# Kernel tuning notes

Measured on AMD Instinct MI355X. Metric: run time of the kernel, lower is better.

Reference implementation:

```python
import jax, jax.numpy as jnp
import numpy as np

N_ENTITIES = 100000
N_RELATIONS = 64
EMBED_DIM = 128
BATCH = 16384
KG_L2_LAMBDA = 1e-05


def setup_inputs() -> dict:
    key = jax.random.key(0)
    ks = jax.random.split(key, 8)
    d = EMBED_DIM
    scale = 1.0 / np.sqrt(d)  # xavier-ish init scale
    return {
        'h': jax.random.randint(ks[0], (BATCH,), 0, N_ENTITIES),
        'r': jax.random.randint(ks[1], (BATCH,), 0, N_RELATIONS),
        'pos_t': jax.random.randint(ks[2], (BATCH,), 0, N_ENTITIES),
        'neg_t': jax.random.randint(ks[3], (BATCH,), 0, N_ENTITIES),
        'entity_embed': jax.random.normal(ks[4], (N_ENTITIES, d), jnp.float32) * scale,
        'relation_embed': jax.random.normal(ks[5], (N_RELATIONS, d), jnp.float32) * scale,
        'h_trans_w1': jnp.ones((d,), jnp.float32),
        'h_trans_w2': jnp.ones((d,), jnp.float32),
        'h_bias_b': jnp.zeros((d,), jnp.float32),
        'r_trans_w1': jnp.ones((d,), jnp.float32),
        'r_trans_w2': jnp.ones((d,), jnp.float32),
        'r_bias_b': jnp.zeros((d,), jnp.float32),
        'sem_trans_w': jax.random.normal(ks[6], (2 * d, d), jnp.float32) * scale,
    }


def _l2_loss_mean(x):
    return jnp.mean(jnp.sum(x * x, axis=1) / 2.0)


def reference(h, r, pos_t, neg_t, entity_embed, relation_embed,
              h_trans_w1, h_trans_w2, h_bias_b,
              r_trans_w1, r_trans_w2, r_bias_b, sem_trans_w):
    h_e = entity_embed[h]          # (B, d)
    r_e = relation_embed[r]        # (B, d)
    pos_t_e = entity_embed[pos_t]  # (B, d)
    neg_t_e = entity_embed[neg_t]  # (B, d)

    # calc_sur: sem[b,i,j] = h_e[b,i] * r_e[b,j]; matmul(sem, w) == h_e * (r_e @ w),
    # matmul(sem^T, w) == r_e * (h_e @ w). Fused form of the same math.
    r_w1 = (r_e @ h_trans_w1)[:, None]
    r_w2 = (r_e @ h_trans_w2)[:, None]
    h_w1 = (h_e @ r_trans_w1)[:, None]
    h_w2 = (h_e @ r_trans_w2)[:, None]
    cross_h = h_e * r_w1 + r_e * h_w2 + h_bias_b  # (B, d)
    cross_r = h_e * r_w2 + r_e * h_w1 + r_bias_b  # (B, d)

    pred_t = jnp.concatenate([cross_h, cross_r], axis=1) @ sem_trans_w  # (B, d)
    pos_score = jnp.sum(pred_t * pos_t_e, axis=1)
    neg_score = jnp.sum(pred_t * neg_t_e, axis=1)
    # -logsigmoid(x) == softplus(-x)
    kg_loss = jnp.mean(jax.nn.softplus(-(pos_score - neg_score)))
    l2_loss = (_l2_loss_mean(cross_h) + _l2_loss_mean(cross_r)
               + _l2_loss_mean(pos_t_e) + _l2_loss_mean(neg_t_e))
    return kg_loss + KG_L2_LAMBDA * l2_loss
```

## Files before the change

### kernel.cpp

```cpp
#include <hip/hip_runtime.h>
#include <hip/hip_bf16.h>

#define B_TOTAL 16384
#define EMB 128
#define NBLK 256
#define TPB 256
#define KG_LAMBDA 1e-5f
#define WT_STRIDE 264
#define IMG_BYTES 73728
#define IMG_DW (IMG_BYTES / 4)
#define WT_DW 16896
#define SVEC_BYTE_OFF 67584

typedef float f32x4 __attribute__((ext_vector_type(4)));
typedef unsigned u32x4 __attribute__((ext_vector_type(4)));
typedef __bf16 bf16x8 __attribute__((ext_vector_type(8)));

__device__ __forceinline__ unsigned pack_bf16x2(float a, float b) {
  unsigned ua = __float_as_uint(a);
  unsigned ub = __float_as_uint(b);
  ua = (ua + 0x7fffu + ((ua >> 16) & 1u)) >> 16;
  ub = (ub + 0x7fffu + ((ub >> 16) & 1u)) >> 16;
  return ua | (ub << 16);
}

__global__ __launch_bounds__(256) void sur_prep(
    const float* __restrict__ W,
    const float* __restrict__ htw1, const float* __restrict__ htw2,
    const float* __restrict__ hbias,
    const float* __restrict__ rtw1, const float* __restrict__ rtw2,
    const float* __restrict__ rbias,
    unsigned* __restrict__ img) {
  const int idx = blockIdx.x * 256 + threadIdx.x;
  if (idx < WT_DW) {
    const int c = idx / 132;
    const int kp = idx - c * 132;
    unsigned v = 0;
    if (kp < 128) {
      const float f0 = W[(2 * kp) * EMB + c];
      const float f1 = W[(2 * kp + 1) * EMB + c];
      v = pack_bf16x2(f0, f1);
    }
    img[idx] = v;
  } else {
    const int j = idx - WT_DW;
    float val = 0.f;
    if (j < 768) {
      const int vsel = j >> 7, cc = j & 127;
      const float* src = vsel == 0 ? htw1 : vsel == 1 ? htw2 : vsel == 2 ? hbias
                       : vsel == 3 ? rtw1 : vsel == 4 ? rtw2 : rbias;
      val = src[cc];
    }
    img[idx] = __float_as_uint(val);
  }
}

__global__ __launch_bounds__(TPB, 2) void sur_fused(
    const int* __restrict__ h, const int* __restrict__ r,
    const int* __restrict__ pos_t, const int* __restrict__ neg_t,
    const float* __restrict__ ent, const float* __restrict__ rel,
    const unsigned* __restrict__ img, float* __restrict__ out) {
  __shared__ __align__(16) unsigned char smem[IMG_BYTES];
  __shared__ float redbuf[2][4];
  unsigned short (*Wt)[WT_STRIDE] = (unsigned short(*)[WT_STRIDE])smem;
  const float* svec = (const float*)(smem + SVEC_BYTE_OFF);

  const int tid = threadIdx.x;
  const int lane = tid & 63;
  const int wave = tid >> 6;
  const int ri = lane & 15;
  const int q = lane >> 4;

  const int rowbase = blockIdx.x * 64 + wave * 16;
  const int hidx = h[rowbase + ri] * EMB;
  const int ridx = r[rowbase + ri] * EMB;
  int pidx[4], nidx[4];
  #pragma unroll
  for (int g = 0; g < 4; ++g) {
    pidx[g] = pos_t[rowbase + q * 4 + g] * EMB;
    nidx[g] = neg_t[rowbase + q * 4 + g] * EMB;
  }

  {
    const float4* gsrc = (const float4*)img;
    float4* ldst = (float4*)smem;
    #pragma unroll
    for (int i = 0; i < IMG_BYTES / 16 / TPB; ++i)
      ldst[i * TPB + tid] = gsrc[i * TPB + tid];
  }

  float he[4][8], re[4][8];
  #pragma unroll
  for (int kt = 0; kt < 4; ++kt) {
    const int c0 = kt * 32 + q * 8;
    const float4 a0 = *reinterpret_cast<const float4*>(ent + hidx + c0);
    const float4 a1 = *reinterpret_cast<const float4*>(ent + hidx + c0 + 4);
    const float4 b0 = *reinterpret_cast<const float4*>(rel + ridx + c0);
    const float4 b1 = *reinterpret_cast<const float4*>(rel + ridx + c0 + 4);
    he[kt][0] = a0.x; he[kt][1] = a0.y; he[kt][2] = a0.z; he[kt][3] = a0.w;
    he[kt][4] = a1.x; he[kt][5] = a1.y; he[kt][6] = a1.z; he[kt][7] = a1.w;
    re[kt][0] = b0.x; re[kt][1] = b0.y; re[kt][2] = b0.z; re[kt][3] = b0.w;
    re[kt][4] = b1.x; re[kt][5] = b1.y; re[kt][6] = b1.z; re[kt][7] = b1.w;
  }

  float pe[4][8], ne[4][8];
  #pragma unroll
  for (int g = 0; g < 4; ++g) {
    #pragma unroll
    for (int n = 0; n < 8; ++n) {
      pe[g][n] = ent[pidx[g] + n * 16 + ri];
      ne[g][n] = ent[nidx[g] + n * 16 + ri];
    }
  }

  __syncthreads();

  float prw1 = 0.f, prw2 = 0.f, phw1 = 0.f, phw2 = 0.f;
  #pragma unroll
  for (int kt = 0; kt < 4; ++kt) {
    const int c0 = kt * 32 + q * 8;
    #pragma unroll
    for (int j = 0; j < 8; ++j) {
      prw1 = fmaf(re[kt][j], svec[0 * 128 + c0 + j], prw1);
      prw2 = fmaf(re[kt][j], svec[1 * 128 + c0 + j], prw2);
      phw1 = fmaf(he[kt][j], svec[3 * 128 + c0 + j], phw1);
      phw2 = fmaf(he[kt][j], svec[4 * 128 + c0 + j], phw2);
    }
  }
  prw1 += __shfl_xor(prw1, 16); prw2 += __shfl_xor(prw2, 16);
  phw1 += __shfl_xor(phw1, 16); phw2 += __shfl_xor(phw2, 16);
  prw1 += __shfl_xor(prw1, 32); prw2 += __shfl_xor(prw2, 32);
  phw1 += __shfl_xor(phw1, 32); phw2 += __shfl_xor(phw2, 32);

  float acc_l2 = 0.f;
  u32x4 afu[8];
  #pragma unroll
  for (int kt = 0; kt < 4; ++kt) {
    const int c0 = kt * 32 + q * 8;
    float ch[8], cr[8];
    #pragma unroll
    for (int j = 0; j < 8; ++j) {
      const float hb = svec[2 * 128 + c0 + j];
      const float rb = svec[5 * 128 + c0 + j];
      ch[j] = fmaf(he[kt][j], prw1, fmaf(re[kt][j], phw2, hb));
      cr[j] = fmaf(he[kt][j], prw2, fmaf(re[kt][j], phw1, rb));
      acc_l2 += ch[j] * ch[j] + cr[j] * cr[j];
    }
    #pragma unroll
    for (int d = 0; d < 4; ++d) {
      afu[kt][d]     = pack_bf16x2(ch[2 * d], ch[2 * d + 1]);
      afu[kt + 4][d] = pack_bf16x2(cr[2 * d], cr[2 * d + 1]);
    }
  }

  f32x4 acc[8];
  #pragma unroll
  for (int n = 0; n < 8; ++n) acc[n] = 0.f;
  #pragma unroll
  for (int t = 0; t < 8; ++t) {
    const bf16x8 av = __builtin_bit_cast(bf16x8, afu[t]);
    #pragma unroll
    for (int n = 0; n < 8; ++n) {
      const bf16x8 bv = *reinterpret_cast<const bf16x8*>(&Wt[n * 16 + ri][t * 32 + q * 8]);
      acc[n] = __builtin_amdgcn_mfma_f32_16x16x32_bf16(av, bv, acc[n], 0, 0, 0);
    }
  }

  float sp[4] = {0.f, 0.f, 0.f, 0.f}, sn[4] = {0.f, 0.f, 0.f, 0.f};
  #pragma unroll
  for (int n = 0; n < 8; ++n) {
    #pragma unroll
    for (int g = 0; g < 4; ++g) {
      sp[g] = fmaf(acc[n][g], pe[g][n], sp[g]);
      sn[g] = fmaf(acc[n][g], ne[g][n], sn[g]);
      acc_l2 += pe[g][n] * pe[g][n] + ne[g][n] * ne[g][n];
    }
  }
  #pragma unroll
  for (int m = 1; m < 16; m <<= 1) {
    #pragma unroll
    for (int g = 0; g < 4; ++g) {
      sp[g] += __shfl_xor(sp[g], m);
      sn[g] += __shfl_xor(sn[g], m);
    }
  }
  float acc_kg = 0.f;
  if (ri == 0) {
    #pragma unroll
    for (int g = 0; g < 4; ++g) {
      const float x = sn[g] - sp[g];
      acc_kg += fmaxf(x, 0.f) + log1pf(expf(-fabsf(x)));
    }
  }

  float kg = acc_kg, l2 = acc_l2;
  #pragma unroll
  for (int m = 1; m < 64; m <<= 1) {
    kg += __shfl_xor(kg, m);
    l2 += __shfl_xor(l2, m);
  }
  if (lane == 0) { redbuf[0][wave] = kg; redbuf[1][wave] = l2; }
  __syncthreads();
  if (tid == 0) {
    const float K = redbuf[0][0] + redbuf[0][1] + redbuf[0][2] + redbuf[0][3];
    const float L = redbuf[1][0] + redbuf[1][1] + redbuf[1][2] + redbuf[1][3];
    atomicAdd(out, (K + KG_LAMBDA * 0.5f * L) * (1.0f / (float)B_TOTAL));
  }
}

extern "C" void kernel_launch(void* const* d_in, const int* in_sizes, int n_in,
                              void* d_out, int out_size, void* d_ws, size_t ws_size,
                              hipStream_t stream) {
  const int* h     = (const int*)d_in[0];
  const int* r     = (const int*)d_in[1];
  const int* pos_t = (const int*)d_in[2];
  const int* neg_t = (const int*)d_in[3];
  const float* ent  = (const float*)d_in[4];
  const float* rel  = (const float*)d_in[5];
  const float* htw1 = (const float*)d_in[6];
  const float* htw2 = (const float*)d_in[7];
  const float* hb   = (const float*)d_in[8];
  const float* rtw1 = (const float*)d_in[9];
  const float* rtw2 = (const float*)d_in[10];
  const float* rb   = (const float*)d_in[11];
  const float* W    = (const float*)d_in[12];
  unsigned* img = (unsigned*)d_ws;
  float* out = (float*)d_out;

  hipMemsetAsync(d_out, 0, sizeof(float), stream);
  hipLaunchKernelGGL(sur_prep, dim3(IMG_DW / 256), dim3(256), 0, stream,
                     W, htw1, htw2, hb, rtw1, rtw2, rb, img);
  hipLaunchKernelGGL(sur_fused, dim3(NBLK), dim3(TPB), 0, stream,
                     h, r, pos_t, neg_t, ent, rel, img, out);
}
```

Baseline: 116.1 us.

## Pre-swizzle weight fragments in global memory and halve rows per wave

The prep kernel now writes the bf16 weight matrix already arranged in per-lane MFMA B-fragment order. The fused kernel reads these fragments directly from global/L2 instead of staging a 72KB shared-memory image behind a barrier. Each wave now handles 8 rows instead of 16, with duplicated rows masked out of the loss sums, and the grid doubles to 512 blocks for more parallelism. The output memset is folded into the prep kernel, removing one launch. In exchange, half of the MFMA rows are redundant and every block re-reads the weights from cache.

```diff
diff --git a/kernel.cpp b/kernel.cpp
--- a/kernel.cpp
+++ b/kernel.cpp
@@ -3,14 +3,13 @@
 
 #define B_TOTAL 16384
 #define EMB 128
-#define NBLK 256
 #define TPB 256
+#define NBLK 512
 #define KG_LAMBDA 1e-5f
-#define WT_STRIDE 264
-#define IMG_BYTES 73728
-#define IMG_DW (IMG_BYTES / 4)
-#define WT_DW 16896
-#define SVEC_BYTE_OFF 67584
+#define FRAG_DW 16384
+#define SVEC_DW 768
+#define IMG_DW (FRAG_DW + SVEC_DW)
+#define PREP_BLOCKS (IMG_DW / 256)
 
 typedef float f32x4 __attribute__((ext_vector_type(4)));
 typedef unsigned u32x4 __attribute__((ext_vector_type(4)));
@@ -30,28 +29,28 @@
     const float* __restrict__ hbias,
     const float* __restrict__ rtw1, const float* __restrict__ rtw2,
     const float* __restrict__ rbias,
-    unsigned* __restrict__ img) {
+    unsigned* __restrict__ img, float* __restrict__ out) {
   const int idx = blockIdx.x * 256 + threadIdx.x;
-  if (idx < WT_DW) {
-    const int c = idx / 132;
-    const int kp = idx - c * 132;
-    unsigned v = 0;
-    if (kp < 128) {
-      const float f0 = W[(2 * kp) * EMB + c];
-      const float f1 = W[(2 * kp + 1) * EMB + c];
-      v = pack_bf16x2(f0, f1);
-    }
-    img[idx] = v;
+  if (idx < FRAG_DW) {
+    const int kp = idx >> 7;
+    const int c  = idx & 127;
+    const float f0 = W[(2 * kp) * EMB + c];
+    const float f1 = W[(2 * kp + 1) * EMB + c];
+    const int t  = kp >> 4;
+    const int rm = kp & 15;
+    const int q8 = rm >> 2;
+    const int w  = rm & 3;
+    const int n  = c >> 4;
+    const int ri = c & 15;
+    const int l  = q8 * 16 + ri;
+    img[((t * 8 + n) << 8) + (l << 2) + w] = pack_bf16x2(f0, f1);
   } else {
-    const int j = idx - WT_DW;
-    float val = 0.f;
-    if (j < 768) {
-      const int vsel = j >> 7, cc = j & 127;
-      const float* src = vsel == 0 ? htw1 : vsel == 1 ? htw2 : vsel == 2 ? hbias
-                       : vsel == 3 ? rtw1 : vsel == 4 ? rtw2 : rbias;
-      val = src[cc];
-    }
-    img[idx] = __float_as_uint(val);
+    const int j = idx - FRAG_DW;
+    const int vsel = j >> 7, cc = j & 127;
+    const float* src = vsel == 0 ? htw1 : vsel == 1 ? htw2 : vsel == 2 ? hbias
+                     : vsel == 3 ? rtw1 : vsel == 4 ? rtw2 : rbias;
+    img[idx] = __float_as_uint(src[cc]);
+    if (j == 0) out[0] = 0.f;
   }
 }
 
@@ -60,10 +59,7 @@
     const int* __restrict__ pos_t, const int* __restrict__ neg_t,
     const float* __restrict__ ent, const float* __restrict__ rel,
     const unsigned* __restrict__ img, float* __restrict__ out) {
-  __shared__ __align__(16) unsigned char smem[IMG_BYTES];
   __shared__ float redbuf[2][4];
-  unsigned short (*Wt)[WT_STRIDE] = (unsigned short(*)[WT_STRIDE])smem;
-  const float* svec = (const float*)(smem + SVEC_BYTE_OFF);
 
   const int tid = threadIdx.x;
   const int lane = tid & 63;
@@ -71,23 +67,20 @@
   const int ri = lane & 15;
   const int q = lane >> 4;
 
-  const int rowbase = blockIdx.x * 64 + wave * 16;
-  const int hidx = h[rowbase + ri] * EMB;
-  const int ridx = r[rowbase + ri] * EMB;
+  const int rowbase = (blockIdx.x * 4 + wave) * 8;
+  const int arow = ri & 7;
+  const int hidx = h[rowbase + arow] * EMB;
+  const int ridx = r[rowbase + arow] * EMB;
+  const int qq = q & 1;
   int pidx[4], nidx[4];
   #pragma unroll
   for (int g = 0; g < 4; ++g) {
-    pidx[g] = pos_t[rowbase + q * 4 + g] * EMB;
-    nidx[g] = neg_t[rowbase + q * 4 + g] * EMB;
-  }
-
-  {
-    const float4* gsrc = (const float4*)img;
-    float4* ldst = (float4*)smem;
-    #pragma unroll
-    for (int i = 0; i < IMG_BYTES / 16 / TPB; ++i)
-      ldst[i * TPB + tid] = gsrc[i * TPB + tid];
-  }
+    const int rr = rowbase + qq * 4 + g;
+    pidx[g] = pos_t[rr] * EMB;
+    nidx[g] = neg_t[rr] * EMB;
+  }
+
+  const float* svec = (const float*)(img + FRAG_DW);
 
   float he[4][8], re[4][8];
   #pragma unroll
@@ -103,28 +96,24 @@
     re[kt][4] = b1.x; re[kt][5] = b1.y; re[kt][6] = b1.z; re[kt][7] = b1.w;
   }
 
-  float pe[4][8], ne[4][8];
-  #pragma unroll
-  for (int g = 0; g < 4; ++g) {
-    #pragma unroll
-    for (int n = 0; n < 8; ++n) {
-      pe[g][n] = ent[pidx[g] + n * 16 + ri];
-      ne[g][n] = ent[nidx[g] + n * 16 + ri];
-    }
-  }
-
-  __syncthreads();
-
   float prw1 = 0.f, prw2 = 0.f, phw1 = 0.f, phw2 = 0.f;
   #pragma unroll
   for (int kt = 0; kt < 4; ++kt) {
     const int c0 = kt * 32 + q * 8;
-    #pragma unroll
-    for (int j = 0; j < 8; ++j) {
-      prw1 = fmaf(re[kt][j], svec[0 * 128 + c0 + j], prw1);
-      prw2 = fmaf(re[kt][j], svec[1 * 128 + c0 + j], prw2);
-      phw1 = fmaf(he[kt][j], svec[3 * 128 + c0 + j], phw1);
-      phw2 = fmaf(he[kt][j], svec[4 * 128 + c0 + j], phw2);
+    const float4 w1a = *reinterpret_cast<const float4*>(svec + 0 * 128 + c0);
+    const float4 w1b = *reinterpret_cast<const float4*>(svec + 0 * 128 + c0 + 4);
+    const float4 w2a = *reinterpret_cast<const float4*>(svec + 1 * 128 + c0);
+    const float4 w2b = *reinterpret_cast<const float4*>(svec + 1 * 128 + c0 + 4);
+    const float4 v1a = *reinterpret_cast<const float4*>(svec + 3 * 128 + c0);
+    const float4 v1b = *reinterpret_cast<const float4*>(svec + 3 * 128 + c0 + 4);
+    const float4 v2a = *reinterpret_cast<const float4*>(svec + 4 * 128 + c0);
+    const float4 v2b = *reinterpret_cast<const float4*>(svec + 4 * 128 + c0 + 4);
+    #pragma unroll
+    for (int j = 0; j < 4; ++j) {
+      prw1 = fmaf(re[kt][j], (&w1a.x)[j], prw1); prw1 = fmaf(re[kt][j + 4], (&w1b.x)[j], prw1);
+      prw2 = fmaf(re[kt][j], (&w2a.x)[j], prw2); prw2 = fmaf(re[kt][j + 4], (&w2b.x)[j], prw2);
+      phw1 = fmaf(he[kt][j], (&v1a.x)[j], phw1); phw1 = fmaf(he[kt][j + 4], (&v1b.x)[j], phw1);
+      phw2 = fmaf(he[kt][j], (&v2a.x)[j], phw2); phw2 = fmaf(he[kt][j + 4], (&v2b.x)[j], phw2);
     }
   }
   prw1 += __shfl_xor(prw1, 16); prw2 += __shfl_xor(prw2, 16);
@@ -132,19 +121,24 @@
   prw1 += __shfl_xor(prw1, 32); prw2 += __shfl_xor(prw2, 32);
   phw1 += __shfl_xor(phw1, 32); phw2 += __shfl_xor(phw2, 32);
 
+  const float m8 = (ri < 8) ? 1.f : 0.f;
   float acc_l2 = 0.f;
   u32x4 afu[8];
   #pragma unroll
   for (int kt = 0; kt < 4; ++kt) {
     const int c0 = kt * 32 + q * 8;
+    const float4 hba = *reinterpret_cast<const float4*>(svec + 2 * 128 + c0);
+    const float4 hbb = *reinterpret_cast<const float4*>(svec + 2 * 128 + c0 + 4);
+    const float4 rba = *reinterpret_cast<const float4*>(svec + 5 * 128 + c0);
+    const float4 rbb = *reinterpret_cast<const float4*>(svec + 5 * 128 + c0 + 4);
     float ch[8], cr[8];
     #pragma unroll
     for (int j = 0; j < 8; ++j) {
-      const float hb = svec[2 * 128 + c0 + j];
-      const float rb = svec[5 * 128 + c0 + j];
+      const float hb = j < 4 ? (&hba.x)[j] : (&hbb.x)[j - 4];
+      const float rb = j < 4 ? (&rba.x)[j] : (&rbb.x)[j - 4];
       ch[j] = fmaf(he[kt][j], prw1, fmaf(re[kt][j], phw2, hb));
       cr[j] = fmaf(he[kt][j], prw2, fmaf(re[kt][j], phw1, rb));
-      acc_l2 += ch[j] * ch[j] + cr[j] * cr[j];
+      acc_l2 = fmaf(m8, ch[j] * ch[j] + cr[j] * cr[j], acc_l2);
     }
     #pragma unroll
     for (int d = 0; d < 4; ++d) {
@@ -153,6 +147,17 @@
     }
   }
 
+  float pe[4][8], ne[4][8];
+  #pragma unroll
+  for (int g = 0; g < 4; ++g) {
+    #pragma unroll
+    for (int n = 0; n < 8; ++n) {
+      pe[g][n] = ent[pidx[g] + n * 16 + ri];
+      ne[g][n] = ent[nidx[g] + n * 16 + ri];
+    }
+  }
+
+  const u32x4* frag = (const u32x4*)img;
   f32x4 acc[8];
   #pragma unroll
   for (int n = 0; n < 8; ++n) acc[n] = 0.f;
@@ -161,11 +166,12 @@
     const bf16x8 av = __builtin_bit_cast(bf16x8, afu[t]);
     #pragma unroll
     for (int n = 0; n < 8; ++n) {
-      const bf16x8 bv = *reinterpret_cast<const bf16x8*>(&Wt[n * 16 + ri][t * 32 + q * 8]);
+      const bf16x8 bv = __builtin_bit_cast(bf16x8, frag[(t * 8 + n) * 64 + lane]);
       acc[n] = __builtin_amdgcn_mfma_f32_16x16x32_bf16(av, bv, acc[n], 0, 0, 0);
     }
   }
 
+  const float mq = (q < 2) ? 1.f : 0.f;
   float sp[4] = {0.f, 0.f, 0.f, 0.f}, sn[4] = {0.f, 0.f, 0.f, 0.f};
   #pragma unroll
   for (int n = 0; n < 8; ++n) {
@@ -173,7 +179,7 @@
     for (int g = 0; g < 4; ++g) {
       sp[g] = fmaf(acc[n][g], pe[g][n], sp[g]);
       sn[g] = fmaf(acc[n][g], ne[g][n], sn[g]);
-      acc_l2 += pe[g][n] * pe[g][n] + ne[g][n] * ne[g][n];
+      acc_l2 = fmaf(mq, pe[g][n] * pe[g][n] + ne[g][n] * ne[g][n], acc_l2);
     }
   }
   #pragma unroll
@@ -185,7 +191,7 @@
     }
   }
   float acc_kg = 0.f;
-  if (ri == 0) {
+  if (ri == 0 && q < 2) {
     #pragma unroll
     for (int g = 0; g < 4; ++g) {
       const float x = sn[g] - sp[g];
@@ -227,9 +233,8 @@
   unsigned* img = (unsigned*)d_ws;
   float* out = (float*)d_out;
 
-  hipMemsetAsync(d_out, 0, sizeof(float), stream);
-  hipLaunchKernelGGL(sur_prep, dim3(IMG_DW / 256), dim3(256), 0, stream,
-                     W, htw1, htw2, hb, rtw1, rtw2, rb, img);
+  hipLaunchKernelGGL(sur_prep, dim3(PREP_BLOCKS), dim3(256), 0, stream,
+                     W, htw1, htw2, hb, rtw1, rtw2, rb, img, out);
   hipLaunchKernelGGL(sur_fused, dim3(NBLK), dim3(TPB), 0, stream,
                      h, r, pos_t, neg_t, ent, rel, img, out);
 }
```

After: 121.2 us. 1.04x slower.

## Halve rows per wave, stage pred in LDS, vectorize tail gathers, fold memset

Applied to the files above, without the earlier changes.

Each wave now handles 8 rows instead of 16. The MFMA runs on duplicated rows and the duplicates are masked out of the L2 sum. The block count doubles so more of the GPU's compute units are busy. Pred tiles are written to shared memory so each lane can load pos/neg entity rows as coalesced float4 segments instead of scalar strided loads. The separate memset is folded into the prep kernel. In exchange, half of the MFMA work is wasted, more shared-memory weight-image copies are made, and extra barriers are added.

```diff
diff --git a/kernel.cpp b/kernel.cpp
--- a/kernel.cpp
+++ b/kernel.cpp
@@ -3,14 +3,15 @@
 
 #define B_TOTAL 16384
 #define EMB 128
-#define NBLK 256
 #define TPB 256
+#define NBLK 512
 #define KG_LAMBDA 1e-5f
 #define WT_STRIDE 264
 #define IMG_BYTES 73728
 #define IMG_DW (IMG_BYTES / 4)
 #define WT_DW 16896
 #define SVEC_BYTE_OFF 67584
+#define PREDL_STRIDE 132
 
 typedef float f32x4 __attribute__((ext_vector_type(4)));
 typedef unsigned u32x4 __attribute__((ext_vector_type(4)));
@@ -30,7 +31,7 @@
     const float* __restrict__ hbias,
     const float* __restrict__ rtw1, const float* __restrict__ rtw2,
     const float* __restrict__ rbias,
-    unsigned* __restrict__ img) {
+    unsigned* __restrict__ img, float* __restrict__ out) {
   const int idx = blockIdx.x * 256 + threadIdx.x;
   if (idx < WT_DW) {
     const int c = idx / 132;
@@ -52,6 +53,7 @@
       val = src[cc];
     }
     img[idx] = __float_as_uint(val);
+    if (j == 0) out[0] = 0.f;
   }
 }
 
@@ -64,22 +66,22 @@
   __shared__ float redbuf[2][4];
   unsigned short (*Wt)[WT_STRIDE] = (unsigned short(*)[WT_STRIDE])smem;
   const float* svec = (const float*)(smem + SVEC_BYTE_OFF);
+  float* predL = (float*)smem;
 
   const int tid = threadIdx.x;
   const int lane = tid & 63;
   const int wave = tid >> 6;
   const int ri = lane & 15;
   const int q = lane >> 4;
-
-  const int rowbase = blockIdx.x * 64 + wave * 16;
-  const int hidx = h[rowbase + ri] * EMB;
-  const int ridx = r[rowbase + ri] * EMB;
-  int pidx[4], nidx[4];
-  #pragma unroll
-  for (int g = 0; g < 4; ++g) {
-    pidx[g] = pos_t[rowbase + q * 4 + g] * EMB;
-    nidx[g] = neg_t[rowbase + q * 4 + g] * EMB;
-  }
+  const int erow = lane >> 3;
+  const int eseg = lane & 7;
+
+  const int rowbase = (blockIdx.x * 4 + wave) * 8;
+  const int arow = ri & 7;
+  const int hidx = h[rowbase + arow] * EMB;
+  const int ridx = r[rowbase + arow] * EMB;
+  const int pp = pos_t[rowbase + erow] * EMB;
+  const int nn = neg_t[rowbase + erow] * EMB;
 
   {
     const float4* gsrc = (const float4*)img;
@@ -103,16 +105,6 @@
     re[kt][4] = b1.x; re[kt][5] = b1.y; re[kt][6] = b1.z; re[kt][7] = b1.w;
   }
 
-  float pe[4][8], ne[4][8];
-  #pragma unroll
-  for (int g = 0; g < 4; ++g) {
-    #pragma unroll
-    for (int n = 0; n < 8; ++n) {
-      pe[g][n] = ent[pidx[g] + n * 16 + ri];
-      ne[g][n] = ent[nidx[g] + n * 16 + ri];
-    }
-  }
-
   __syncthreads();
 
   float prw1 = 0.f, prw2 = 0.f, phw1 = 0.f, phw2 = 0.f;
@@ -132,6 +124,7 @@
   prw1 += __shfl_xor(prw1, 32); prw2 += __shfl_xor(prw2, 32);
   phw1 += __shfl_xor(phw1, 32); phw2 += __shfl_xor(phw2, 32);
 
+  const float m8 = (ri < 8) ? 1.f : 0.f;
   float acc_l2 = 0.f;
   u32x4 afu[8];
   #pragma unroll
@@ -144,7 +137,7 @@
       const float rb = svec[5 * 128 + c0 + j];
       ch[j] = fmaf(he[kt][j], prw1, fmaf(re[kt][j], phw2, hb));
       cr[j] = fmaf(he[kt][j], prw2, fmaf(re[kt][j], phw1, rb));
-      acc_l2 += ch[j] * ch[j] + cr[j] * cr[j];
+      acc_l2 = fmaf(m8, ch[j] * ch[j] + cr[j] * cr[j], acc_l2);
     }
     #pragma unroll
     for (int d = 0; d < 4; ++d) {
@@ -166,31 +159,46 @@
     }
   }
 
-  float sp[4] = {0.f, 0.f, 0.f, 0.f}, sn[4] = {0.f, 0.f, 0.f, 0.f};
-  #pragma unroll
-  for (int n = 0; n < 8; ++n) {
-    #pragma unroll
-    for (int g = 0; g < 4; ++g) {
-      sp[g] = fmaf(acc[n][g], pe[g][n], sp[g]);
-      sn[g] = fmaf(acc[n][g], ne[g][n], sn[g]);
-      acc_l2 += pe[g][n] * pe[g][n] + ne[g][n] * ne[g][n];
-    }
-  }
-  #pragma unroll
-  for (int m = 1; m < 16; m <<= 1) {
-    #pragma unroll
-    for (int g = 0; g < 4; ++g) {
-      sp[g] += __shfl_xor(sp[g], m);
-      sn[g] += __shfl_xor(sn[g], m);
-    }
-  }
+  float4 pe4[4], ne4[4];
+  #pragma unroll
+  for (int j = 0; j < 4; ++j) {
+    pe4[j] = *reinterpret_cast<const float4*>(ent + pp + eseg * 16 + j * 4);
+    ne4[j] = *reinterpret_cast<const float4*>(ent + nn + eseg * 16 + j * 4);
+  }
+
+  __syncthreads();
+
+  float* myPred = predL + wave * (8 * PREDL_STRIDE);
+  if (q < 2) {
+    #pragma unroll
+    for (int n = 0; n < 8; ++n) {
+      #pragma unroll
+      for (int g = 0; g < 4; ++g)
+        myPred[(q * 4 + g) * PREDL_STRIDE + n * 16 + ri] = acc[n][g];
+    }
+  }
+  __syncthreads();
+
+  float sp = 0.f, sn = 0.f;
+  #pragma unroll
+  for (int j = 0; j < 4; ++j) {
+    const float4 pr = *reinterpret_cast<const float4*>(
+        myPred + erow * PREDL_STRIDE + eseg * 16 + j * 4);
+    sp += pr.x * pe4[j].x + pr.y * pe4[j].y + pr.z * pe4[j].z + pr.w * pe4[j].w;
+    sn += pr.x * ne4[j].x + pr.y * ne4[j].y + pr.z * ne4[j].z + pr.w * ne4[j].w;
+    acc_l2 += pe4[j].x * pe4[j].x + pe4[j].y * pe4[j].y
+            + pe4[j].z * pe4[j].z + pe4[j].w * pe4[j].w
+            + ne4[j].x * ne4[j].x + ne4[j].y * ne4[j].y
+            + ne4[j].z * ne4[j].z + ne4[j].w * ne4[j].w;
+  }
+  sp += __shfl_xor(sp, 1); sn += __shfl_xor(sn, 1);
+  sp += __shfl_xor(sp, 2); sn += __shfl_xor(sn, 2);
+  sp += __shfl_xor(sp, 4); sn += __shfl_xor(sn, 4);
+
   float acc_kg = 0.f;
-  if (ri == 0) {
-    #pragma unroll
-    for (int g = 0; g < 4; ++g) {
-      const float x = sn[g] - sp[g];
-      acc_kg += fmaxf(x, 0.f) + log1pf(expf(-fabsf(x)));
-    }
+  if (eseg == 0) {
+    const float x = sn - sp;
+    acc_kg = fmaxf(x, 0.f) + log1pf(expf(-fabsf(x)));
   }
 
   float kg = acc_kg, l2 = acc_l2;
@@ -227,9 +235,8 @@
   unsigned* img = (unsigned*)d_ws;
   float* out = (float*)d_out;
 
-  hipMemsetAsync(d_out, 0, sizeof(float), stream);
   hipLaunchKernelGGL(sur_prep, dim3(IMG_DW / 256), dim3(256), 0, stream,
-                     W, htw1, htw2, hb, rtw1, rtw2, rb, img);
+                     W, htw1, htw2, hb, rtw1, rtw2, rb, img, out);
   hipLaunchKernelGGL(sur_fused, dim3(NBLK), dim3(TPB), 0, stream,
                      h, r, pos_t, neg_t, ent, rel, img, out);
 }
```

Result: no change. 118.3 us (+2.0%).
